# Kernel tuning notes

Hardware: AMD Instinct MI355X
Metric: run time of the kernel (lower is better)

## Reference

```python
import jax, jax.numpy as jnp
import numpy as np

H, HD, NKV = 16, 128, 4           # heads, head_dim, n_kv_heads (kv_groups=4)
SEL_TOPK, SEL_DIM, SEL_HEADS = 64, 64, 1
ROPE_BASE = 10000.0


def _rope_emb(t, hd):
    inv = 1.0 / (ROPE_BASE ** (jnp.arange(0, hd, 2, dtype=jnp.float32) / hd))
    freqs = jnp.arange(t, dtype=jnp.float32)[:, None] * inv[None, :]
    return jnp.concatenate([freqs, freqs], axis=-1)  # [t, hd]


def _apply_rotary(x, rope):
    # x: [b, t, h, hd]; rope: [t, hd] (rot_dim == hd here)
    cos = jnp.cos(rope)[None, :, None, :]
    sin = jnp.sin(rope)[None, :, None, :]
    x1, x2 = x[..., ::2], x[..., 1::2]
    c, s = cos[..., ::2], sin[..., ::2]
    rot = jnp.stack([x1 * c - x2 * s, x1 * s + x2 * c], axis=-1)
    return rot.reshape(x.shape)


def _selector_mask(q, k):
    # q, k: [b, H, t, hd] in UNrotated form (selector_rope='none'); causal=True
    b, h, t, d = q.shape
    qs = q[:, :SEL_HEADS, :, :SEL_DIM]
    ks = k[:, :SEL_HEADS, :, :SEL_DIM]
    scores = jnp.einsum('bhqd,bhkd->bhqk', qs, ks) / np.sqrt(SEL_DIM).astype(np.float32)
    future = jnp.triu(jnp.ones((t, t), bool), 1)
    scores = jnp.where(future[None, None], -jnp.inf, scores)
    idx = jax.lax.top_k(scores, SEL_TOPK)[1]  # [b, h_sel, t, keep]
    rows = jnp.arange(t)
    scatter_row = lambda im: jnp.zeros((t, t), bool).at[rows[:, None], im].set(True)
    sel = jax.vmap(jax.vmap(scatter_row))(idx)          # [b, h_sel, t, t]
    sel = sel.at[:, :, rows, rows].set(True)            # diagonal always kept
    sel = sel & jnp.tril(jnp.ones((t, t), bool))[None, None]
    sel = jnp.any(sel, axis=1, keepdims=True)           # h_sel < h -> broadcast mask
    return jnp.where(sel, 0.0, -jnp.inf).astype(jnp.float32)


def reference(x, Wq, bq, Wkd, bkd, Wku, bku, Wo, bo):
    b, t, d = x.shape
    G = H // NKV
    q = (x @ Wq + bq).reshape(b, t, H, HD)
    kv = (x @ Wkd + bkd) @ Wku + bku                    # MLA: down then up projection
    k = kv[..., : NKV * HD].reshape(b, t, NKV, HD)
    v = kv[..., NKV * HD:].reshape(b, t, NKV, HD)
    rope = _rope_emb(t, HD)
    qb = _apply_rotary(q, rope).transpose(0, 2, 1, 3)                     # [b,H,t,hd]
    kb = jnp.repeat(_apply_rotary(k, rope).transpose(0, 2, 1, 3), G, 1)   # GQA expand
    vb = jnp.repeat(v.transpose(0, 2, 1, 3), G, 1)
    # selector mask from unrotated q/k, detached (selector_detach=True)
    qu = jax.lax.stop_gradient(q.transpose(0, 2, 1, 3))
    ku = jnp.repeat(jax.lax.stop_gradient(k.transpose(0, 2, 1, 3)), G, 1)
    mask = _selector_mask(qu, ku)                                         # [b,1,t,t]
    scores = jnp.einsum('bhqd,bhkd->bhqk', qb, kb) / np.sqrt(HD).astype(np.float32)
    attn = jax.nn.softmax(scores + mask, axis=-1)
    y = jnp.einsum('bhqk,bhkd->bhqd', attn, vb)
    y = y.transpose(0, 2, 1, 3).reshape(b, t, H * HD)
    return y @ Wo + bo


def setup_inputs() -> dict:
    key = jax.random.key(0)
    ks = jax.random.split(key, 6)
    B, T, D, LAT = 2, 2048, 2048, 512
    s = 0.02
    return {
        'x': jax.random.normal(ks[0], (B, T, D), jnp.float32),
        'Wq': jax.random.normal(ks[1], (D, H * HD), jnp.float32) * s,
        'bq': jnp.zeros((H * HD,), jnp.float32),
        'Wkd': jax.random.normal(ks[2], (D, LAT), jnp.float32) * s,
        'bkd': jnp.zeros((LAT,), jnp.float32),
        'Wku': jax.random.normal(ks[3], (LAT, 2 * NKV * HD), jnp.float32) * s,
        'bku': jnp.zeros((2 * NKV * HD,), jnp.float32),
        'Wo': jax.random.normal(ks[4], (H * HD, D), jnp.float32) * s,
        'bo': jnp.zeros((D,), jnp.float32),
    }
```

## Files before the change

kernel.cpp:

```cpp
#include <hip/hip_runtime.h>

typedef unsigned int u32;
typedef unsigned long long u64;
typedef _Float16 f16;
typedef __attribute__((ext_vector_type(2))) _Float16 f16x2;
typedef __attribute__((ext_vector_type(4))) _Float16 f16x4;
typedef __attribute__((ext_vector_type(8))) _Float16 f16x8;
typedef __attribute__((ext_vector_type(4))) float f32x4;
typedef __attribute__((ext_vector_type(2))) double f64x2;


__device__ __forceinline__ int suX(int jj) { return jj ^ ((jj >> 4) & 7); }

__device__ __forceinline__ void dev_transpose_cast(char* smem, int bx, int by,
                                                   const float* __restrict__ in,
                                                   f16* __restrict__ out, int R, int C)
{
  float* tile = (float*)smem;
  int c0 = bx * 32, r0 = by * 32;
  int tx = threadIdx.x & 31, ty = threadIdx.x >> 5;
  #pragma unroll
  for (int i = ty; i < 32; i += 8) tile[i * 33 + tx] = in[(size_t)(r0 + i) * C + c0 + tx];
  __syncthreads();
  #pragma unroll
  for (int i = ty; i < 32; i += 8) out[(size_t)(c0 + i) * R + r0 + tx] = (f16)tile[tx * 33 + i];
}

__global__ __launch_bounds__(256) void k_fusedP(const float* __restrict__ Wq, f16* __restrict__ WqT,
                                                const float* __restrict__ Wkd, f16* __restrict__ WkdT,
                                                const float* __restrict__ Wku, f16* __restrict__ WkuT,
                                                const float* __restrict__ Wo, f16* __restrict__ WoT,
                                                const float* __restrict__ x, f16* __restrict__ xh)
{
  __shared__ __align__(16) char smem[4224];
  const int id = blockIdx.x;
  if (id < 4096) {
    dev_transpose_cast(smem, id & 63, id >> 6, Wq, WqT, 2048, 2048);
  } else if (id < 5120) {
    int g = id - 4096;
    dev_transpose_cast(smem, g & 15, g >> 4, Wkd, WkdT, 2048, 512);
  } else if (id < 5632) {
    int g = id - 5120;
    dev_transpose_cast(smem, g & 31, g >> 5, Wku, WkuT, 512, 1024);
  } else if (id < 9728) {
    int g = id - 5632;
    dev_transpose_cast(smem, g & 63, g >> 6, Wo, WoT, 2048, 2048);
  } else {
    int i = (id - 9728) * 256 + threadIdx.x;
    f32x4 v = *(const f32x4*)&x[(size_t)i * 4];
    f16x4 h; h.x = (f16)v.x; h.y = (f16)v.y; h.z = (f16)v.z; h.w = (f16)v.w;
    *(f16x4*)&xh[(size_t)i * 4] = h;
  }
}

__global__ void k_prep_sel(const float* __restrict__ Wq, const float* __restrict__ Wkd,
                           const float* __restrict__ Wku, double* __restrict__ Bsel)
{
  const int k = blockIdx.x;
  const int j = threadIdx.x;
  Bsel[(size_t)k * 128 + j] = (double)Wq[(size_t)k * 2048 + j];
  double s = 0.0;
  for (int l = 0; l < 512; ++l)
    s = fma((double)Wkd[(size_t)k * 512 + l], (double)Wku[(size_t)l * 1024 + j], s);
  Bsel[(size_t)k * 128 + 64 + j] = s;
}

__global__ void k_bias_sel(const float* __restrict__ bq, const float* __restrict__ bkd,
                           const float* __restrict__ Wku, const float* __restrict__ bku,
                           double* __restrict__ bsel)
{
  int j = threadIdx.x;
  if (j < 64) {
    bsel[j] = (double)bq[j];
  } else {
    int jj = j - 64;
    double s = (double)bku[jj];
    for (int l = 0; l < 512; ++l)
      s = fma((double)bkd[l], (double)Wku[(size_t)l * 1024 + jj], s);
    bsel[j] = s;
  }
}

__device__ __forceinline__ void dev_sel_f64(char* smem, int bx, int by, int bz,
                                            const float* __restrict__ A,
                                            const double* __restrict__ Bsel,
                                            double* __restrict__ partial)
{
  double* Asd = (double*)smem;
  double* Bsd = (double*)smem + 32 * 33;
  const int m0 = bx * 32, n0 = by * 64;
  const int kbase = bz * 256, kend = kbase + 256;
  const int tid = threadIdx.x;
  const int tx = tid & 15, ty = tid >> 4;
  const int ar = tid >> 3, ac4 = (tid & 7) * 4;
  double acc[2][4] = {};

  f32x4 aN = *(const f32x4*)&A[(size_t)(m0 + ar) * 2048 + kbase + ac4];
  f64x2 bN[4];
  #pragma unroll
  for (int it = 0; it < 4; ++it) {
    int c = it * 256 + tid; int kk = c >> 5, n2 = (c & 31) * 2;
    bN[it] = *(const f64x2*)&Bsel[(size_t)(kbase + kk) * 128 + n0 + n2];
  }
  for (int k0 = kbase; k0 < kend; k0 += 32) {
    __syncthreads();
    Asd[ar * 33 + ac4] = (double)aN.x; Asd[ar * 33 + ac4 + 1] = (double)aN.y;
    Asd[ar * 33 + ac4 + 2] = (double)aN.z; Asd[ar * 33 + ac4 + 3] = (double)aN.w;
    #pragma unroll
    for (int it = 0; it < 4; ++it) {
      int c = it * 256 + tid; int kk = c >> 5, n2 = (c & 31) * 2;
      Bsd[kk * 66 + n2] = bN[it].x; Bsd[kk * 66 + n2 + 1] = bN[it].y;
    }
    __syncthreads();
    if (k0 + 32 < kend) {
      aN = *(const f32x4*)&A[(size_t)(m0 + ar) * 2048 + k0 + 32 + ac4];
      #pragma unroll
      for (int it = 0; it < 4; ++it) {
        int c = it * 256 + tid; int kk = c >> 5, n2 = (c & 31) * 2;
        bN[it] = *(const f64x2*)&Bsel[(size_t)(k0 + 32 + kk) * 128 + n0 + n2];
      }
    }
    #pragma unroll
    for (int kk = 0; kk < 32; ++kk) {
      double a0 = Asd[(ty * 2) * 33 + kk], a1 = Asd[(ty * 2 + 1) * 33 + kk];
      f64x2 b01 = *(const f64x2*)&Bsd[kk * 66 + tx * 2];
      f64x2 b23 = *(const f64x2*)&Bsd[kk * 66 + tx * 2 + 32];
      acc[0][0] = fma(a0, b01.x, acc[0][0]); acc[0][1] = fma(a0, b01.y, acc[0][1]);
      acc[0][2] = fma(a0, b23.x, acc[0][2]); acc[0][3] = fma(a0, b23.y, acc[0][3]);
      acc[1][0] = fma(a1, b01.x, acc[1][0]); acc[1][1] = fma(a1, b01.y, acc[1][1]);
      acc[1][2] = fma(a1, b23.x, acc[1][2]); acc[1][3] = fma(a1, b23.y, acc[1][3]);
    }
  }
  double* op = partial + (size_t)bz * 4096 * 128;
  #pragma unroll
  for (int i = 0; i < 2; ++i) {
    int row = m0 + ty * 2 + i;
    #pragma unroll
    for (int j = 0; j < 2; ++j) {
      op[(size_t)row * 128 + n0 + tx * 2 + j] = acc[i][j];
      op[(size_t)row * 128 + n0 + tx * 2 + 32 + j] = acc[i][j + 2];
    }
  }
}

__device__ __forceinline__ void dev_sel_reduce(int blk,
                                               const double* __restrict__ partial,
                                               const double* __restrict__ bias,
                                               double* __restrict__ qs64,
                                               double* __restrict__ ks64)
{
  const int idx = blk * 256 + threadIdx.x;
  const int row = idx >> 7, n = idx & 127;
  const size_t S = 4096 * 128;
  double v = partial[idx];
  #pragma unroll
  for (int z = 1; z < 8; ++z) v += partial[(size_t)z * S + idx];
  v += bias[n];
  if (n < 64) qs64[(size_t)row * 64 + n] = v;
  else        ks64[(size_t)row * 64 + (n - 64)] = v;
}

__global__ __launch_bounds__(256) void k_transpose64(const double* __restrict__ in,
                                                     double* __restrict__ out)
{
  __shared__ double tile[32][33];
  const int bt = blockIdx.z;
  const int c0 = blockIdx.x * 32;
  const int r0 = blockIdx.y * 32;
  int tx = threadIdx.x & 31, ty = threadIdx.x >> 5;
  const double* ip = in + (size_t)bt * 2048 * 64;
  double* op = out + (size_t)bt * 64 * 2048;
  #pragma unroll
  for (int i = ty; i < 32; i += 8) tile[i][tx] = ip[(size_t)(r0 + i) * 64 + c0 + tx];
  __syncthreads();
  #pragma unroll
  for (int i = ty; i < 32; i += 8) op[(size_t)(c0 + i) * 2048 + r0 + tx] = tile[tx][i];
}

template <int MODE>
__device__ __forceinline__ void dev_gemm_bt(char* smem, int gbx, int gby, int nbx, int nby,
                                            const f16* __restrict__ A,
                                            const f16* __restrict__ BT,
                                            const float* __restrict__ bias,
                                            float* __restrict__ C, f16* __restrict__ Ch,
                                            f16* __restrict__ Kout, f16* __restrict__ Vout,
                                            const float* __restrict__ rc,
                                            const float* __restrict__ rs,
                                            int K, int lda, int ldb, int ldc)
{
  f16* As = (f16*)smem;
  f16* Bs = (f16*)smem + 128 * 64;
  const int tid = threadIdx.x;
  const int lane = tid & 63;
  const int wave = tid >> 6;
  int bx = gbx, by = gby;
  {
    const int nwg = nbx * nby;
    if ((nwg & 7) == 0) {
      const int bid = by * nbx + bx;
      const int cpx = nwg >> 3;
      const int sbid = (bid & 7) * cpx + (bid >> 3);
      bx = sbid % nbx;
      by = sbid / nbx;
    }
  }
  const int m0 = bx * 128, n0 = by * 64;
  const int wr = (wave >> 1) * 64, wc = (wave & 1) * 32;
  const int lrow = lane & 15;
  const int kgrp = (lane >> 4) * 8;
  f32x4 acc[4][2] = {};

  for (int k0 = 0; k0 < K; k0 += 64) {
    __syncthreads();
    #pragma unroll
    for (int it = 0; it < 4; ++it) {
      int c = it * 256 + tid;
      int r = c >> 3, c8 = (c & 7) * 8;
      int lbase = (it * 256 + (tid & 192)) * 8;
      const f16* ga = A + (size_t)(m0 + r) * lda + k0 + c8;
      __builtin_amdgcn_global_load_lds((const __attribute__((address_space(1))) u32*)ga,
                                       (__attribute__((address_space(3))) u32*)&As[lbase],
                                       16, 0, 0);
    }
    #pragma unroll
    for (int it = 0; it < 2; ++it) {
      int c = it * 256 + tid;
      int r = c >> 3, c8 = (c & 7) * 8;
      int lbase = (it * 256 + (tid & 192)) * 8;
      const f16* gb = BT + (size_t)(n0 + r) * ldb + k0 + c8;
      __builtin_amdgcn_global_load_lds((const __attribute__((address_space(1))) u32*)gb,
                                       (__attribute__((address_space(3))) u32*)&Bs[lbase],
                                       16, 0, 0);
    }
    __syncthreads();
    #pragma unroll
    for (int ks = 0; ks < 2; ++ks) {
      f16x8 af[4], bfr[2];
      #pragma unroll
      for (int m = 0; m < 4; ++m)
        af[m] = *(const f16x8*)&As[(wr + m * 16 + lrow) * 64 + ks * 32 + kgrp];
      #pragma unroll
      for (int n = 0; n < 2; ++n)
        bfr[n] = *(const f16x8*)&Bs[(wc + n * 16 + lrow) * 64 + ks * 32 + kgrp];
      #pragma unroll
      for (int m = 0; m < 4; ++m)
        #pragma unroll
        for (int n = 0; n < 2; ++n)
          acc[m][n] = __builtin_amdgcn_mfma_f32_16x16x32_f16(af[m], bfr[n], acc[m][n], 0, 0, 0);
    }
  }
  const int rbase = m0 + wr + (lane >> 4) * 4;
  #pragma unroll
  for (int n = 0; n < 2; ++n) {
    int col = n0 + wc + n * 16 + lrow;
    float bv = bias ? bias[col] : 0.0f;
    const int ri = (col & 127) >> 1;
    #pragma unroll
    for (int m = 0; m < 4; ++m) {
      #pragma unroll
      for (int j = 0; j < 4; ++j) {
        int rowi = rbase + m * 16 + j;
        float v = acc[m][n][j] + bv;
        if (MODE == 0) {
          C[(size_t)rowi * ldc + col] = v;
        } else if (MODE == 1) {
          Ch[(size_t)rowi * ldc + col] = (f16)v;
        } else if (MODE == 2) {
          float vp = __shfl_xor(v, 1);
          int t = rowi & 2047;
          float c_ = rc[t * 64 + ri], s_ = rs[t * 64 + ri];
          float r_ = (lrow & 1) ? (vp * s_ + v * c_) : (v * c_ - vp * s_);
          Ch[(size_t)rowi * ldc + col] = (f16)r_;
        } else {
          float vp = __shfl_xor(v, 1);
          if (n0 < 512) {
            int t = rowi & 2047;
            float c_ = rc[t * 64 + ri], s_ = rs[t * 64 + ri];
            float r_ = (lrow & 1) ? (vp * s_ + v * c_) : (v * c_ - vp * s_);
            Kout[(size_t)rowi * 512 + col] = (f16)r_;
          } else {
            Vout[(size_t)rowi * 512 + (col - 512)] = (f16)v;
          }
        }
      }
    }
  }
}

__global__ void k_rope_table(float* __restrict__ rc, float* __restrict__ rs)
{
  int t = blockIdx.x, i = threadIdx.x;
  int fi = (2 * i) & 63;
  double inv = pow(10000.0, -(double)fi / 64.0);
  double a = (double)t * inv;
  rc[t * 64 + i] = (float)cos(a);
  rs[t * 64 + i] = (float)sin(a);
}

__global__ __launch_bounds__(512) void k_topk(const double* __restrict__ qs,
                                              const double* __restrict__ ksT,
                                              int* __restrict__ selcnt,
                                              int* __restrict__ selidx)
{
  const int r0 = blockIdx.x * 2;
  const int b = r0 >> 11;
  const int t0 = r0 & 2047, t1 = t0 + 1;
  const int tid = threadIdx.x;
  const int lane = tid & 63, wave = tid >> 6;
  if (t1 < 64) {
    for (int lr = 0; lr < 2; ++lr) {
      int t = t0 + lr;
      int* outp = selidx + (size_t)(r0 + lr) * 68;
      for (int jj = tid; jj <= t; jj += 512) outp[jj] = jj;
      if (tid == 0) selcnt[r0 + lr] = t + 1;
    }
    return;
  }
  __shared__ double qrowP[64][2];
  __shared__ u64 su[2][2048];
  __shared__ unsigned hist[256];
  __shared__ unsigned wsum[8];
  __shared__ unsigned s_bsel, s_larger, s_cnt;
  __shared__ u64 s_thr;
  __shared__ int s_remfin;
  __shared__ int cand[128];
  __shared__ u64 ckey[128];

  if (tid < 128) qrowP[tid >> 1][tid & 1] = qs[(size_t)(r0 + (tid & 1)) * 64 + (tid >> 1)];
  __syncthreads();
  {
    const double* kb = ksT + (size_t)b * 64 * 2048;
    const int emax = t1 >> 9;
    for (int e = 0; e <= emax; ++e) {
      const int jj = e * 512 + tid;
      const double* kp = kb + jj;
      double a0 = 0.0, a1 = 0.0, b0 = 0.0, b1 = 0.0;
      #pragma unroll 8
      for (int d = 0; d < 64; d += 2) {
        double kv0 = kp[(size_t)d * 2048];
        double kv1 = kp[(size_t)(d + 1) * 2048];
        f64x2 qp0 = *(const f64x2*)&qrowP[d][0];
        f64x2 qp1 = *(const f64x2*)&qrowP[d + 1][0];
        a0 = fma(qp0.x, kv0, a0); a1 = fma(qp0.y, kv0, a1);
        b0 = fma(qp1.x, kv1, b0); b1 = fma(qp1.y, kv1, b1);
      }
      const int sx = suX(jj);
      u64 u0 = (u64)__double_as_longlong(a0 + b0);
      su[0][sx] = (u0 >> 63) ? ~u0 : (u0 | 0x8000000000000000ull);
      u64 u1 = (u64)__double_as_longlong(a1 + b1);
      su[1][sx] = (u1 >> 63) ? ~u1 : (u1 | 0x8000000000000000ull);
    }
  }
  __syncthreads();

  const int c0 = tid * 4;
  for (int lr = 0; lr < 2; ++lr) {
    const int t = t0 + lr;
    int* outp = selidx + (size_t)(r0 + lr) * 68;
    const u64* S = su[lr];
    u64 kv[4]; bool kvv[4];
    #pragma unroll
    for (int e = 0; e < 4; ++e) {
      const int jj = c0 + e;
      kvv[e] = (jj <= t);
      kv[e] = kvv[e] ? S[suX(jj)] : 0;
    }
    const int nval = (c0 <= t) ? ((c0 + 3 <= t) ? 4 : (t - c0 + 1)) : 0;

    u64 prefix = 0;
    int remaining = 64;
    int broke = 0, sh_final = 0;
    for (int byte = 7; byte >= 0; --byte) {
      const int sh = byte * 8;
      if (tid < 256) hist[tid] = 0;
      __syncthreads();
      {
        unsigned bn[4]; bool vl[4];
        #pragma unroll
        for (int e = 0; e < 4; ++e) {
          vl[e] = kvv[e] && ((byte == 7) || (((kv[e] ^ prefix) >> (sh + 8)) == 0));
          bn[e] = (unsigned)((kv[e] >> sh) & 255);
        }
        unsigned myBin = 0xFFFFFFFFu, cntLoc = 0;
        bool localSame = true;
        #pragma unroll
        for (int e = 0; e < 4; ++e) {
          if (vl[e]) {
            if (myBin == 0xFFFFFFFFu) myBin = bn[e];
            else if (bn[e] != myBin) localSame = false;
            ++cntLoc;
          }
        }
        const bool hasValid = (cntLoc > 0);
        unsigned vmin = hasValid ? myBin : 0xFFFFFFFFu;
        unsigned vmax = hasValid ? myBin : 0u;
        unsigned csum = cntLoc;
        #pragma unroll
        for (int off = 32; off; off >>= 1) {
          unsigned a = __shfl_xor(vmin, off); vmin = a < vmin ? a : vmin;
          unsigned bmx = __shfl_xor(vmax, off); vmax = bmx > vmax ? bmx : vmax;
          csum += __shfl_xor(csum, off);
        }
        const bool anyMixed = (__ballot(hasValid && !localSame) != 0ull);
        const bool anyValid = (__ballot(hasValid) != 0ull);
        if (!anyMixed && anyValid && vmin == vmax) {
          if (lane == 0) atomicAdd(&hist[vmin], csum);
        } else if (hasValid) {
          #pragma unroll
          for (int e = 0; e < 4; ++e) {
            if (vl[e]) {
              bool first = true;
              #pragma unroll
              for (int p = 0; p < 4; ++p)
                if (p < e && vl[p] && bn[p] == bn[e]) first = false;
              if (first) {
                unsigned c = 0;
                #pragma unroll
                for (int q = 0; q < 4; ++q)
                  if (q >= e && vl[q] && bn[q] == bn[e]) ++c;
                atomicAdd(&hist[bn[e]], c);
              }
            }
          }
        }
      }
      __syncthreads();
      unsigned inc = 0, cumAbove = 0;
      if (tid < 256) {
        const unsigned h = hist[tid];
        unsigned v = h;
        #pragma unroll
        for (int off = 1; off < 64; off <<= 1) {
          unsigned tv = __shfl_down(v, off);
          if (lane + off < 64) v += tv;
        }
        if (lane == 0) wsum[wave] = v;
        inc = v; cumAbove = h;
      }
      __syncthreads();
      if (tid < 256) {
        unsigned add = 0;
        #pragma unroll
        for (int w = 0; w < 4; ++w)
          if (w > wave) add += wsum[w];
        const unsigned h = cumAbove;
        inc += add;
        cumAbove = inc - h;
      }
      __syncthreads();
      if (tid < 256 && (int)cumAbove < remaining && (int)inc >= remaining) {
        s_bsel = (unsigned)tid;
        s_larger = cumAbove;
        s_cnt = inc - cumAbove;
      }
      __syncthreads();
      prefix |= ((u64)s_bsel << sh);
      remaining -= (int)s_larger;
      int cnt = (int)s_cnt;
      if (cnt <= 128) { broke = 1; sh_final = sh; break; }
    }
    u64 thr;
    int remfin;
    if (broke) {
      unsigned cg = 0;
      #pragma unroll
      for (int e = 0; e < 4; ++e)
        if (kvv[e] && (((kv[e] ^ prefix) >> sh_final) == 0)) ++cg;
      unsigned v = cg;
      #pragma unroll
      for (int off = 1; off < 64; off <<= 1) {
        unsigned tv = __shfl_up(v, off);
        if (lane >= off) v += tv;
      }
      __syncthreads();
      if (lane == 63) wsum[wave] = v;
      __syncthreads();
      unsigned add = 0, tot = 0;
      #pragma unroll
      for (int w = 0; w < 8; ++w) {
        tot += wsum[w];
        if (w < wave) add += wsum[w];
      }
      const int C = (int)tot;
      int pos = (int)(v + add - cg);
      __syncthreads();
      #pragma unroll
      for (int e = 0; e < 4; ++e)
        if (kvv[e] && (((kv[e] ^ prefix) >> sh_final) == 0)) cand[pos++] = c0 + e;
      __syncthreads();
      if (tid < C) ckey[tid] = S[suX(cand[tid])];
      __syncthreads();
      if (tid < C) {
        u64 k = ckey[tid];
        int g = 0, eq = 0;
        for (int j = 0; j < C; ++j) {
          g += (ckey[j] > k) ? 1 : 0;
          eq += (ckey[j] == k) ? 1 : 0;
        }
        if (g < remaining && remaining <= g + eq) {
          s_thr = k;
          s_remfin = remaining - g;
        }
      }
      __syncthreads();
      thr = s_thr;
      remfin = s_remfin;
    } else {
      thr = prefix;
      remfin = remaining;
    }
    __syncthreads();
    unsigned cg = 0, ct_ = 0;
    #pragma unroll
    for (int e = 0; e < 4; ++e) {
      if (kvv[e]) {
        cg += (kv[e] > thr) ? 1u : 0u;
        ct_ += (kv[e] == thr) ? 1u : 0u;
      }
    }
    const unsigned pack = cg | (ct_ << 16);
    {
      unsigned v = pack;
      #pragma unroll
      for (int off = 1; off < 64; off <<= 1) {
        unsigned tv = __shfl_up(v, off);
        if (lane >= off) v += tv;
      }
      if (lane == 63) wsum[wave] = v;
      __syncthreads();
      unsigned add = 0, tot = 0;
      #pragma unroll
      for (int w = 0; w < 8; ++w) {
        tot += wsum[w];
        if (w < wave) add += wsum[w];
      }
      const unsigned excl = v + add - pack;
      __syncthreads();
      const unsigned Gtot = tot & 0xFFFFu;
      const u64 ut = S[suX(t)];
      const unsigned gt = (ut > thr) ? 1u : 0u;
      const unsigned tt = (ut == thr) ? 1u : 0u;
      const int GtotX = (int)(Gtot - gt);
      int gpos = (int)(excl & 0xFFFFu);
      int tpos = (int)(excl >> 16);
      #pragma unroll
      for (int e = 0; e < 4; ++e) {
        const int jj = c0 + e;
        if (!kvv[e]) break;
        if (kv[e] > thr) {
          if (jj != t) outp[1 + gpos] = jj;
          ++gpos;
        } else if (kv[e] == thr) {
          if (jj != t && tpos < remfin) outp[1 + GtotX + tpos] = jj;
          ++tpos;
        }
      }
      if (tid == 0) {
        outp[0] = t;
        const unsigned Ttot = tot >> 16;
        int tb = (int)(Ttot - tt);
        int emitT = tb < remfin ? tb : remfin;
        selcnt[r0 + lr] = 1 + GtotX + emitT;
      }
    }
    __syncthreads();
  }
}

__global__ __launch_bounds__(256) void k_fusedA(const float* __restrict__ x,
                                                const double* __restrict__ Bsel,
                                                double* __restrict__ partial,
                                                const f16* __restrict__ xh,
                                                const f16* __restrict__ WkdT,
                                                const float* __restrict__ bkd,
                                                f16* __restrict__ cbf)
{
  __shared__ __align__(16) char smem[25600];
  const int id = blockIdx.x;
  if (id < 2048) {
    dev_sel_f64(smem, id & 127, (id >> 7) & 1, id >> 8, x, Bsel, partial);
  } else {
    const int g = id - 2048;
    dev_gemm_bt<1>(smem, g & 31, g >> 5, 32, 8, xh, WkdT, bkd, nullptr, cbf,
                   nullptr, nullptr, nullptr, nullptr, 2048, 2048, 2048, 512);
  }
}

__global__ __launch_bounds__(256) void k_fusedC(const f16* __restrict__ cbf,
                                                const f16* __restrict__ WkuT,
                                                const float* __restrict__ bku,
                                                f16* __restrict__ krope, f16* __restrict__ vbf,
                                                const float* __restrict__ rc,
                                                const float* __restrict__ rs,
                                                const double* __restrict__ partial,
                                                const double* __restrict__ bsel,
                                                double* __restrict__ qs64,
                                                double* __restrict__ ks64)
{
  __shared__ __align__(16) char smem[24576];
  const int id = blockIdx.x;
  if (id < 512) {
    dev_gemm_bt<3>(smem, id & 31, id >> 5, 32, 16, cbf, WkuT, bku, nullptr, nullptr,
                   krope, vbf, rc, rs, 512, 512, 512, 1024);
  } else {
    dev_sel_reduce(id - 512, partial, bsel, qs64, ks64);
  }
}

__global__ __launch_bounds__(256) void k_gemmQ(const f16* __restrict__ xh,
                                               const f16* __restrict__ WqT,
                                               const float* __restrict__ bq,
                                               f16* __restrict__ qrope,
                                               const float* __restrict__ rc,
                                               const float* __restrict__ rs)
{
  __shared__ __align__(16) char smem[24576];
  dev_gemm_bt<2>(smem, blockIdx.x, blockIdx.y, 32, 32, xh, WqT, bq, nullptr, qrope,
                 nullptr, nullptr, rc, rs, 2048, 2048, 2048, 2048);
}

__global__ __launch_bounds__(256) void k_gemmO(const f16* __restrict__ A,
                                               const f16* __restrict__ BT,
                                               const float* __restrict__ bias,
                                               float* __restrict__ C)
{
  __shared__ __align__(16) char smem[24576];
  dev_gemm_bt<0>(smem, blockIdx.x, blockIdx.y, 32, 32, A, BT, bias, C, nullptr,
                 nullptr, nullptr, nullptr, nullptr, 2048, 2048, 2048, 2048);
}

__global__ __launch_bounds__(256) void k_attn(const f16* __restrict__ qr,
                                              const f16* __restrict__ kr,
                                              const f16* __restrict__ vv,
                                              const int* __restrict__ selcnt,
                                              const int* __restrict__ selidx,
                                              f16* __restrict__ y)
{
  const int blk = blockIdx.x;
  const int row = blk >> 2, kvh = blk & 3;
  const int b = row >> 11;
  const int tid = threadIdx.x, lane = tid & 63, wave = tid >> 6;
  const int cnt = selcnt[row];
  __shared__ int sidx[68];
  __shared__ __align__(16) f16 Kl[65 * 128];
  __shared__ __align__(16) f16 Vl[68 * 128];
  __shared__ f16 qlds[4][128];
  __shared__ __align__(4) f16 ph[4][72];
  if (tid < cnt) sidx[tid] = selidx[(size_t)row * 68 + tid];
  *(f16x2*)&qlds[wave][lane * 2] =
      *(const f16x2*)&qr[((size_t)row * 16 + kvh * 4 + wave) * 128 + lane * 2];
  __syncthreads();

  f16x8 kreg[5], vreg[5];
  int rr[5], cc[5]; bool vld[5];
  #pragma unroll
  for (int it = 0; it < 5; ++it) {
    const int c = it * 256 + tid;
    const int r = c >> 4, ch = c & 15;
    const bool ok = (r < cnt);
    const int rsafe = ok ? sidx[r] : sidx[0];
    const size_t kbase = ((size_t)(b * 2048 + rsafe)) * 512 + kvh * 128 + ch * 8;
    kreg[it] = *(const f16x8*)&kr[kbase];
    vreg[it] = *(const f16x8*)&vv[kbase];
    rr[it] = r; cc[it] = ch; vld[it] = ok;
  }
  #pragma unroll
  for (int it = 0; it < 5; ++it) {
    if (vld[it]) {
      *(f16x8*)&Kl[rr[it] * 128 + ((cc[it] ^ (rr[it] & 15)) * 8)] = kreg[it];
      *(f16x8*)&Vl[rr[it] * 128 + cc[it] * 8] = vreg[it];
    }
  }
  for (int i = tid; i < (68 - cnt) * 64; i += 256)
    ((u32*)Vl)[cnt * 64 + i] = 0u;
  __syncthreads();

  const float SCALE = 0.08838834764831845f;
  auto dotk = [&](int r) -> float {
    const int sw = r & 15;
    float s = 0.0f;
    #pragma unroll
    for (int i = 0; i < 16; ++i) {
      f16x8 k8 = *(const f16x8*)&Kl[r * 128 + ((i ^ sw) * 8)];
      f16x8 q8 = *(const f16x8*)&qlds[wave][i * 8];
      #pragma unroll
      for (int e = 0; e < 4; ++e) {
        f16x2 ka; ka.x = k8[2 * e]; ka.y = k8[2 * e + 1];
        f16x2 qa; qa.x = q8[2 * e]; qa.y = q8[2 * e + 1];
        s = __builtin_amdgcn_fdot2(ka, qa, s, false);
      }
    }
    return s * SCALE;
  };

  float s1 = -__builtin_inff(), s2 = -__builtin_inff();
  if (lane < cnt) s1 = dotk(lane);
  if (lane + 64 < cnt) s2 = dotk(lane + 64);
  float mx = fmaxf(s1, s2);
  #pragma unroll
  for (int off = 32; off; off >>= 1) mx = fmaxf(mx, __shfl_xor(mx, off));
  float p1 = (lane < cnt) ? __expf(s1 - mx) : 0.0f;
  float p2 = (lane + 64 < cnt) ? __expf(s2 - mx) : 0.0f;
  float l = p1 + p2;
  #pragma unroll
  for (int off = 32; off; off >>= 1) l += __shfl_xor(l, off);
  float linv = 1.0f / l;
  ph[wave][lane] = (f16)p1;
  if (lane == 0) ph[wave][64] = (f16)p2;
  if (lane >= 1 && lane < 8) ph[wave][64 + lane] = (f16)0.f;
  __syncthreads();

  float y0 = 0.0f, y1 = 0.0f;
  const int d2 = lane * 2;
  for (int j = 0; j < cnt; j += 2) {
    f16x2 pp = *(const f16x2*)&ph[wave][j];
    f16x2 va = *(const f16x2*)&Vl[(j + 0) * 128 + d2];
    f16x2 vb = *(const f16x2*)&Vl[(j + 1) * 128 + d2];
    f16x2 v0; v0.x = va.x; v0.y = vb.x;
    f16x2 v1; v1.x = va.y; v1.y = vb.y;
    y0 = __builtin_amdgcn_fdot2(pp, v0, y0, false);
    y1 = __builtin_amdgcn_fdot2(pp, v1, y1, false);
  }
  y0 *= linv; y1 *= linv;
  f16x2 o; o.x = (f16)y0; o.y = (f16)y1;
  *(f16x2*)&y[(size_t)row * 2048 + (kvh * 4 + wave) * 128 + d2] = o;
}

extern "C" void kernel_launch(void* const* d_in, const int* in_sizes, int n_in,
                              void* d_out, int out_size, void* d_ws, size_t ws_size,
                              hipStream_t stream)
{
  (void)in_sizes; (void)n_in; (void)out_size; (void)ws_size;
  const float* x   = (const float*)d_in[0];
  const float* Wq  = (const float*)d_in[1];
  const float* bq  = (const float*)d_in[2];
  const float* Wkd = (const float*)d_in[3];
  const float* bkd = (const float*)d_in[4];
  const float* Wku = (const float*)d_in[5];
  const float* bku = (const float*)d_in[6];
  const float* Wo  = (const float*)d_in[7];
  const float* bo  = (const float*)d_in[8];
  float* out = (float*)d_out;

  char* ws = (char*)d_ws;
  size_t o = 0;
  auto alloc = [&](size_t bytes) -> void* {
    o = (o + 255) & ~(size_t)255;
    void* p = ws + o;
    o += bytes;
    return p;
  };
  f16* WqT   = (f16*)alloc(2048ull * 2048 * 2);
  f16* WoT   = (f16*)alloc(2048ull * 2048 * 2);
  f16* WkdT  = (f16*)alloc(512ull * 2048 * 2);
  f16* WkuT  = (f16*)alloc(1024ull * 512 * 2);
  f16* xh    = (f16*)alloc(4096ull * 2048 * 2);
  f16* yh    = (f16*)alloc(4096ull * 2048 * 2);
  f16* cbf   = (f16*)alloc(4096ull * 512 * 2);
  float* rc  = (float*)alloc(2048ull * 64 * 4);
  float* rs  = (float*)alloc(2048ull * 64 * 4);
  f16* qrope = (f16*)alloc(4096ull * 2048 * 2);
  f16* krope = (f16*)alloc(4096ull * 512 * 2);
  f16* vbf   = (f16*)alloc(4096ull * 512 * 2);
  int* selcnt = (int*)alloc(4096ull * 4);
  int* selidx = (int*)alloc(4096ull * 68 * 4);
  double* Bsel = (double*)alloc(2048ull * 128 * 8);
  double* bsel = (double*)alloc(128 * 8);
  double* qs64 = (double*)alloc(4096ull * 64 * 8);
  double* ks64 = (double*)alloc(4096ull * 64 * 8);
  double* ksT  = (double*)alloc(2ull * 64 * 2048 * 8);
  double* partial = (double*)alloc(8ull * 4096 * 128 * 8);

  k_prep_sel<<<2048, 64, 0, stream>>>(Wq, Wkd, Wku, Bsel);
  k_bias_sel<<<1, 128, 0, stream>>>(bq, bkd, Wku, bku, bsel);
  k_rope_table<<<2048, 64, 0, stream>>>(rc, rs);
  k_fusedP<<<17920, 256, 0, stream>>>(Wq, WqT, Wkd, WkdT, Wku, WkuT, Wo, WoT, x, xh);

  k_fusedA<<<2304, 256, 0, stream>>>(x, Bsel, partial, xh, WkdT, bkd, cbf);

  k_fusedC<<<2560, 256, 0, stream>>>(cbf, WkuT, bku, krope, vbf, rc, rs,
                                     partial, bsel, qs64, ks64);

  k_transpose64<<<dim3(2, 64, 2), 256, 0, stream>>>(ks64, ksT);

  k_gemmQ<<<dim3(32, 32), 256, 0, stream>>>(xh, WqT, bq, qrope, rc, rs);
  k_topk<<<2048, 512, 0, stream>>>(qs64, ksT, selcnt, selidx);

  k_attn<<<16384, 256, 0, stream>>>(qrope, krope, vbf, selcnt, selidx, yh);

  k_gemmO<<<dim3(32, 32), 256, 0, stream>>>(yh, WoT, bo, out);
}
```

Measured before the change: 489.7 us.

## Split selector scoring into a register-tiled fp64 GEMM kernel before top-k

Selector score computation moves out of the top-k kernel into a separate k_score kernel. It processes 32 query rows per block against 512 keys, reusing each loaded key column across 32 rows held in registers. The old path re-read the full key matrix for every pair of rows. The scores are written as sortable u64 keys to a new 64MB global buffer, which k_select then reloads. This trades far less redundant key reading and better FMA reuse for extra global write and read traffic, plus one more launch.

```diff
diff --git a/kernel.cpp b/kernel.cpp
--- a/kernel.cpp
+++ b/kernel.cpp
@@ -175,6 +175,49 @@
   __syncthreads();
   #pragma unroll
   for (int i = ty; i < 32; i += 8) op[(size_t)(c0 + i) * 2048 + r0 + tx] = tile[tx][i];
+}
+
+__global__ __launch_bounds__(256) void k_score(const double* __restrict__ qs,
+                                               const double* __restrict__ ksT,
+                                               u64* __restrict__ su)
+{
+  const int rt = blockIdx.x >> 2;
+  const int kc = blockIdx.x & 3;
+  const int tmax = ((rt & 63) << 5) + 31;
+  if (kc * 512 > tmax) return;
+  const int b = rt >> 6;
+  const int tid = threadIdx.x;
+  __shared__ double As[32 * 64];
+  {
+    const double* qp = qs + (size_t)rt * 32 * 64;
+    #pragma unroll
+    for (int i = 0; i < 8; ++i) As[tid * 8 + i] = qp[tid * 8 + i];
+  }
+  __syncthreads();
+  const int k0 = kc * 512 + tid;
+  const int k1 = k0 + 256;
+  const double* kb = ksT + (size_t)b * 64 * 2048;
+  double acc0[32] = {}, acc1[32] = {};
+  for (int d = 0; d < 64; ++d) {
+    const double b0 = kb[(size_t)d * 2048 + k0];
+    const double b1 = kb[(size_t)d * 2048 + k1];
+    #pragma unroll
+    for (int r = 0; r < 32; ++r) {
+      const double a = As[r * 64 + d];
+      acc0[r] = fma(a, b0, acc0[r]);
+      acc1[r] = fma(a, b1, acc1[r]);
+    }
+  }
+  #pragma unroll
+  for (int r = 0; r < 32; ++r) {
+    const int row = rt * 32 + r;
+    u64 u0 = (u64)__double_as_longlong(acc0[r]);
+    u0 = (u0 >> 63) ? ~u0 : (u0 | 0x8000000000000000ull);
+    su[(size_t)row * 2048 + k0] = u0;
+    u64 u1 = (u64)__double_as_longlong(acc1[r]);
+    u1 = (u1 >> 63) ? ~u1 : (u1 | 0x8000000000000000ull);
+    su[(size_t)row * 2048 + k1] = u1;
+  }
 }
 
 template <int MODE>
@@ -297,13 +340,11 @@
   rs[t * 64 + i] = (float)sin(a);
 }
 
-__global__ __launch_bounds__(512) void k_topk(const double* __restrict__ qs,
-                                              const double* __restrict__ ksT,
-                                              int* __restrict__ selcnt,
-                                              int* __restrict__ selidx)
+__global__ __launch_bounds__(512) void k_select(const u64* __restrict__ gsu,
+                                                int* __restrict__ selcnt,
+                                                int* __restrict__ selidx)
 {
   const int r0 = blockIdx.x * 2;
-  const int b = r0 >> 11;
   const int t0 = r0 & 2047, t1 = t0 + 1;
   const int tid = threadIdx.x;
   const int lane = tid & 63, wave = tid >> 6;
@@ -316,7 +357,6 @@
     }
     return;
   }
-  __shared__ double qrowP[64][2];
   __shared__ u64 su[2][2048];
   __shared__ unsigned hist[256];
   __shared__ unsigned wsum[8];
@@ -326,29 +366,13 @@
   __shared__ int cand[128];
   __shared__ u64 ckey[128];
 
-  if (tid < 128) qrowP[tid >> 1][tid & 1] = qs[(size_t)(r0 + (tid & 1)) * 64 + (tid >> 1)];
-  __syncthreads();
   {
-    const double* kb = ksT + (size_t)b * 64 * 2048;
-    const int emax = t1 >> 9;
-    for (int e = 0; e <= emax; ++e) {
-      const int jj = e * 512 + tid;
-      const double* kp = kb + jj;
-      double a0 = 0.0, a1 = 0.0, b0 = 0.0, b1 = 0.0;
-      #pragma unroll 8
-      for (int d = 0; d < 64; d += 2) {
-        double kv0 = kp[(size_t)d * 2048];
-        double kv1 = kp[(size_t)(d + 1) * 2048];
-        f64x2 qp0 = *(const f64x2*)&qrowP[d][0];
-        f64x2 qp1 = *(const f64x2*)&qrowP[d + 1][0];
-        a0 = fma(qp0.x, kv0, a0); a1 = fma(qp0.y, kv0, a1);
-        b0 = fma(qp1.x, kv1, b0); b1 = fma(qp1.y, kv1, b1);
-      }
+    const u64* g0 = gsu + (size_t)r0 * 2048;
+    const u64* g1 = gsu + (size_t)(r0 + 1) * 2048;
+    for (int jj = tid; jj <= t1; jj += 512) {
       const int sx = suX(jj);
-      u64 u0 = (u64)__double_as_longlong(a0 + b0);
-      su[0][sx] = (u0 >> 63) ? ~u0 : (u0 | 0x8000000000000000ull);
-      u64 u1 = (u64)__double_as_longlong(a1 + b1);
-      su[1][sx] = (u1 >> 63) ? ~u1 : (u1 | 0x8000000000000000ull);
+      if (jj <= t0) su[0][sx] = g0[jj];
+      su[1][sx] = g1[jj];
     }
   }
   __syncthreads();
@@ -365,7 +389,6 @@
       kvv[e] = (jj <= t);
       kv[e] = kvv[e] ? S[suX(jj)] : 0;
     }
-    const int nval = (c0 <= t) ? ((c0 + 3 <= t) ? 4 : (t - c0 + 1)) : 0;
 
     u64 prefix = 0;
     int remaining = 64;
@@ -770,6 +793,7 @@
   double* ks64 = (double*)alloc(4096ull * 64 * 8);
   double* ksT  = (double*)alloc(2ull * 64 * 2048 * 8);
   double* partial = (double*)alloc(8ull * 4096 * 128 * 8);
+  u64* gsu = (u64*)alloc(4096ull * 2048 * 8);
 
   k_prep_sel<<<2048, 64, 0, stream>>>(Wq, Wkd, Wku, Bsel);
   k_bias_sel<<<1, 128, 0, stream>>>(bq, bkd, Wku, bku, bsel);
@@ -782,9 +806,10 @@
                                      partial, bsel, qs64, ks64);
 
   k_transpose64<<<dim3(2, 64, 2), 256, 0, stream>>>(ks64, ksT);
+  k_score<<<512, 256, 0, stream>>>(qs64, ksT, gsu);
 
   k_gemmQ<<<dim3(32, 32), 256, 0, stream>>>(xh, WqT, bq, qrope, rc, rs);
-  k_topk<<<2048, 512, 0, stream>>>(qs64, ksT, selcnt, selidx);
+  k_select<<<2048, 512, 0, stream>>>(gsu, selcnt, selidx);
 
   k_attn<<<16384, 256, 0, stream>>>(qrope, krope, vbf, selcnt, selidx, yh);
 
```

Result: no change. 492.4 us (+0.6%).
